# Optimization experiments

Hardware: AMD Instinct MI355X
Metric: run time of the kernel (lower is better)

The kernel has to match this reference:

```python
import jax, jax.numpy as jnp
import numpy as np

N_U, N_P, E = 200000, 50000, 500000
D_U, D_P, H, OUT = 100, 50, 128, 1
BN_EPS = 1e-5


def _lin(k, dout, din):
    s = 1.0 / np.sqrt(din)
    kw, kb = jax.random.split(k)
    W = jax.random.uniform(kw, (dout, din), jnp.float32, -s, s)
    b = jax.random.uniform(kb, (dout,), jnp.float32, -s, s)
    return W, b


def setup_inputs() -> dict:
    key = jax.random.key(0)
    ks = jax.random.split(key, 12)
    x_u = jax.random.normal(ks[0], (N_U, D_U), jnp.float32)
    x_p = jax.random.normal(ks[1], (N_P, D_P), jnp.float32)
    src = jax.random.randint(ks[2], (E,), 0, N_U, jnp.int64) if jax.config.jax_enable_x64 else jax.random.randint(ks[2], (E,), 0, N_U)
    dst = jax.random.randint(ks[3], (E,), N_U, N_U + N_P)
    edge_index = jnp.stack([src, dst]).astype(jnp.int32)
    W_u, b_u = _lin(ks[4], H, D_U)
    W_p, b_p = _lin(ks[5], H, D_P)
    W1l, b1l = _lin(ks[6], H, H)   # SAGEConv lin_l (aggregated neighbors, carries bias)
    W1r, _ = _lin(ks[7], H, H)     # SAGEConv lin_r (root, no bias)
    W2l, b2l = _lin(ks[8], H, H)
    W2r, _ = _lin(ks[9], H, H)
    W_out, b_out = _lin(ks[10], OUT, H)
    return dict(x_u=x_u, x_p=x_p, edge_index=edge_index,
                W_u=W_u, b_u=b_u, W_p=W_p, b_p=b_p,
                W1l=W1l, b1l=b1l, W1r=W1r,
                g1=jnp.ones((H,), jnp.float32), be1=jnp.zeros((H,), jnp.float32),
                W2l=W2l, b2l=b2l, W2r=W2r,
                g2=jnp.ones((H,), jnp.float32), be2=jnp.zeros((H,), jnp.float32),
                W_out=W_out, b_out=b_out)


def reference(x_u, x_p, edge_index, W_u, b_u, W_p, b_p,
              W1l, b1l, W1r, g1, be1, W2l, b2l, W2r, g2, be2,
              W_out, b_out):
    N = x_u.shape[0] + x_p.shape[0]
    # input projections + relu, then concat users/products -> [N, H]
    x = jnp.concatenate([jax.nn.relu(x_u @ W_u.T + b_u),
                         jax.nn.relu(x_p @ W_p.T + b_p)], axis=0)
    # to_undirected: add reversed edges (bipartite => no duplicates)
    src = jnp.concatenate([edge_index[0], edge_index[1]])
    dst = jnp.concatenate([edge_index[1], edge_index[0]])
    deg = jnp.maximum(jax.ops.segment_sum(jnp.ones_like(dst, jnp.float32), dst, num_segments=N), 1.0)

    def sage(h, Wl, bl, Wr):
        # mean aggregation of neighbor features, scatter by dst
        mean = jax.ops.segment_sum(h[src], dst, num_segments=N) / deg[:, None]
        return mean @ Wl.T + bl + h @ Wr.T

    def bn(h, g, b):
        m = h.mean(0)
        v = h.var(0)  # biased variance, as used for normalization in torch BN
        return (h - m) * jax.lax.rsqrt(v + BN_EPS) * g + b

    h1 = jax.nn.relu(bn(sage(x, W1l, b1l, W1r), g1, be1))   # dropout = identity (eval)
    h2 = jax.nn.relu(bn(sage(h1, W2l, b2l, W2r), g2, be2)) + x
    return h2[: x_u.shape[0]] @ W_out.T + b_out
```

## Files before the change

kernel.cpp:

```cpp
#include <hip/hip_runtime.h>
#include <hip/hip_bf16.h>
#include <cstdint>
#include <cstddef>

#define NT   250000
#define NUU  200000
#define NPP  50000
#define EG   500000
#define E2   1000000
#define HD   128
#define NBLK_SCAN 977

#define CNT2_OFF   0ull
#define SPART2_OFF 1000000ull
#define SS2_OFF    1065536ull
#define RPTR2_OFF  1067584ull
#define BSUM2_OFF  2067588ull
#define BMAT2_OFF  2071504ull
#define COL2_OFF   2251728ull
#define X2_OFF     6251728ull
#define R1B_OFF    70251728ull
#define R2B_OFF    134251728ull
#define WS_SPLIT   198251728ull

typedef __hip_bfloat16 bf16;
typedef __attribute__((ext_vector_type(8))) short short8v;
typedef __attribute__((ext_vector_type(4))) float f32x4;

__device__ inline float b2f(short s) { return __builtin_bit_cast(float, ((unsigned)(unsigned short)s) << 16); }
__device__ inline unsigned short f2bf(float f) { return __builtin_bit_cast(unsigned short, __float2bfloat16(f)); }

__global__ __launch_bounds__(256) void k_zero(int* __restrict__ p, int n) {
    for (int i = blockIdx.x * 256 + threadIdx.x; i < n; i += gridDim.x * 256) p[i] = 0;
}

__global__ __launch_bounds__(256) void k_count(const int* __restrict__ ei, int* __restrict__ cnt) {
    for (int e = blockIdx.x * 256 + threadIdx.x; e < EG; e += gridDim.x * 256) {
        int s = ei[e], d = ei[e + EG];
        atomicAdd(&cnt[d], 1);
        atomicAdd(&cnt[s], 1);
    }
}

__global__ __launch_bounds__(256) void k_scan1(const int* __restrict__ cnt, int* __restrict__ bsum) {
    __shared__ int lds[256];
    int i = blockIdx.x * 256 + threadIdx.x;
    int v = (i < NT) ? cnt[i] : 0;
    lds[threadIdx.x] = v; __syncthreads();
    for (int s = 128; s > 0; s >>= 1) {
        if (threadIdx.x < s) lds[threadIdx.x] += lds[threadIdx.x + s];
        __syncthreads();
    }
    if (threadIdx.x == 0) bsum[blockIdx.x] = lds[0];
}

__global__ __launch_bounds__(1024) void k_scan2(int* __restrict__ bsum) {
    __shared__ int lds[1024];
    int i = threadIdx.x;
    int v = (i < NBLK_SCAN) ? bsum[i] : 0;
    lds[i] = v; __syncthreads();
    for (int off = 1; off < 1024; off <<= 1) {
        int t = (i >= off) ? lds[i - off] : 0;
        __syncthreads();
        lds[i] += t;
        __syncthreads();
    }
    if (i < NBLK_SCAN) bsum[i] = lds[i] - v;
}

__global__ __launch_bounds__(256) void k_scan3(const int* __restrict__ cnt, const int* __restrict__ bsum,
                                               int* __restrict__ rp) {
    __shared__ int lds[256];
    int i = blockIdx.x * 256 + threadIdx.x;
    int v = (i < NT) ? cnt[i] : 0;
    lds[threadIdx.x] = v; __syncthreads();
    for (int off = 1; off < 256; off <<= 1) {
        int t = (threadIdx.x >= off) ? lds[threadIdx.x - off] : 0;
        __syncthreads();
        lds[threadIdx.x] += t;
        __syncthreads();
    }
    if (i < NT) rp[i] = bsum[blockIdx.x] + lds[threadIdx.x] - v;
    if (i == 0 && blockIdx.x == 0) rp[NT] = E2;
}

__global__ __launch_bounds__(256) void k_fill(const int* __restrict__ ei, const int* __restrict__ rp,
                                              int* __restrict__ fill, int* __restrict__ col) {
    for (int e = blockIdx.x * 256 + threadIdx.x; e < EG; e += gridDim.x * 256) {
        int s = ei[e], d = ei[e + EG];
        int slot1 = rp[d] + atomicAdd(&fill[d], 1);
        col[slot1] = s;
        int slot2 = rp[s] + atomicAdd(&fill[s], 1);
        col[slot2] = d;
    }
}

__global__ __launch_bounds__(256) void k_wcvt(const float* __restrict__ W1l, const float* __restrict__ W1r,
                                              const float* __restrict__ W2l, const float* __restrict__ W2r,
                                              const float* __restrict__ Wu, const float* __restrict__ Wp,
                                              bf16* __restrict__ B) {
    int i = blockIdx.x * 256 + threadIdx.x;
    if (i < 65536) {
        int layer = i >> 15, rem = i & 32767, o = rem >> 8, k = rem & 255;
        const float* W = layer ? ((k < 128) ? W2l : W2r) : ((k < 128) ? W1l : W1r);
        B[i] = __float2bfloat16(W[o * 128 + (k & 127)]);
    } else if (i < 81920) {
        int rem = i - 65536, o = rem >> 7, k = rem & 127;
        B[i] = __float2bfloat16((k < 100) ? Wu[o * 100 + k] : 0.f);
    } else if (i < 90112) {
        int rem = i - 81920, o = rem >> 6, k = rem & 63;
        B[i] = __float2bfloat16((k < 50) ? Wp[o * 50 + k] : 0.f);
    }
}

template<int DIN, int KPAD>
__device__ __forceinline__ void proj_tile(char* As, const float* __restrict__ in,
                                          const bf16* __restrict__ Bp, const float* __restrict__ bias,
                                          bf16* __restrict__ outp, int nrows, int rowbase, int bid) {
    const int tid = threadIdx.x;
    const int tb = bid * 128;
    constexpr int RSTRIDE = KPAD * 2;
    constexpr int PADE = KPAD - DIN;
    constexpr int PH = PADE / 2;
    constexpr int PPAD = 128 * PH;
    constexpr int PMAIN = 128 * DIN / 2;

    for (int q = tid; q < PPAD; q += 256) {
        int row = q / PH;
        int k = DIN + (q - row * PH) * 2;
        *(unsigned*)(As + row * RSTRIDE + ((((k >> 3) << 4) ^ ((row & 7) << 4)) + (k & 7) * 2)) = 0u;
    }
    for (int q = tid; q < PMAIN; q += 256) {
        int f = q * 2;
        int row = f / DIN, k = f - row * DIN;
        int rg = tb + row; if (rg > nrows - 1) rg = nrows - 1;
        float2 v = *(const float2*)(in + (size_t)rg * DIN + k);
        unsigned u = (unsigned)f2bf(v.x) | ((unsigned)f2bf(v.y) << 16);
        *(unsigned*)(As + row * RSTRIDE + ((((k >> 3) << 4) ^ ((row & 7) << 4)) + (k & 7) * 2)) = u;
    }
    __syncthreads();

    const int lane = tid & 63, wid = tid >> 6;
    const int wr = wid >> 1, wc = wid & 1;
    const int r15 = lane & 15, l4 = lane >> 4;
    constexpr int NKS = KPAD / 32;
    f32x4 acc[4][4] = {};
#pragma unroll
    for (int ks = 0; ks < NKS; ks++) {
        short8v a[4], b[4];
#pragma unroll
        for (int m = 0; m < 4; m++) {
            int rl = wr * 64 + m * 16 + r15;
            a[m] = *(const short8v*)(As + rl * RSTRIDE + ((ks * 64 + l4 * 16) ^ ((rl & 7) << 4)));
        }
#pragma unroll
        for (int n = 0; n < 4; n++) {
            int c = wc * 64 + n * 16 + r15;
            b[n] = *(const short8v*)(Bp + (size_t)c * KPAD + ks * 32 + l4 * 8);
        }
#pragma unroll
        for (int m = 0; m < 4; m++)
#pragma unroll
            for (int n = 0; n < 4; n++)
                acc[m][n] = __builtin_amdgcn_mfma_f32_16x16x32_bf16(a[m], b[n], acc[m][n], 0, 0, 0);
    }
    float bcol[4];
#pragma unroll
    for (int n = 0; n < 4; n++) bcol[n] = bias[wc * 64 + n * 16 + r15];
#pragma unroll
    for (int m = 0; m < 4; m++)
#pragma unroll
        for (int n = 0; n < 4; n++)
#pragma unroll
            for (int g = 0; g < 4; g++) {
                int row = tb + wr * 64 + m * 16 + l4 * 4 + g;
                if (row < nrows) {
                    float v = fmaxf(acc[m][n][g] + bcol[n], 0.f);
                    outp[(size_t)(rowbase + row) * HD + wc * 64 + n * 16 + r15] = __float2bfloat16(v);
                }
            }
}

__global__ __launch_bounds__(256) void k_proj2(const float* __restrict__ xu, const float* __restrict__ xp,
                                               const bf16* __restrict__ Bm, const float* __restrict__ bu,
                                               const float* __restrict__ bp, bf16* __restrict__ X) {
    __shared__ __align__(16) char As[32768];
    if (blockIdx.x < 1563)
        proj_tile<100, 128>(As, xu, Bm + 65536, bu, X, NUU, 0, blockIdx.x);
    else
        proj_tile<50, 64>(As, xp, Bm + 81920, bp, X, NPP, NUU, blockIdx.x - 1563);
}

template<bool NORM>
__global__ __launch_bounds__(256) void k_layer(const bf16* __restrict__ hin, const float* __restrict__ ssv,
                                               const int* __restrict__ rp, const int* __restrict__ col,
                                               const bf16* __restrict__ Bmat, const float* __restrict__ blv,
                                               bf16* __restrict__ outp, float* __restrict__ spart,
                                               int store_n) {
    int g = blockIdx.x / 5, pos = blockIdx.x % 5;
    int tile = (pos < 4) ? (g * 4 + pos) : (1563 + g);
    if (pos < 4 && tile > 1562) return;

    __shared__ __align__(16) char At[32768];
    __shared__ int rpl[129];
    __shared__ int ctr;
    const int tid = threadIdx.x;
    const int tb = tile * 128;

    if (tid < 129) rpl[tid] = rp[min(tb + tid, NT)];
    if (tid == 255) ctr = 0;
    __syncthreads();

    const int lane = tid & 63;
    const int l8 = tid & 7;
    const int fo = l8 * 8;
    float sva[8], tva[8], svb[8], tvb[8];
    if (NORM) {
#pragma unroll
        for (int j = 0; j < 8; j++) {
            sva[j] = ssv[fo + j];      tva[j] = ssv[HD + fo + j];
            svb[j] = ssv[64 + fo + j]; tvb[j] = ssv[HD + 64 + fo + j];
        }
    }
    for (;;) {
        int nl = 0;
        if (l8 == 0) nl = atomicAdd(&ctr, 1);
        nl = __shfl(nl, lane & 56);
        if (nl >= 128) break;
        int s0 = rpl[nl], s1 = rpl[nl + 1];
        float a[8] = {}, b[8] = {};
        for (int p = s0; p < s1; p += 4) {
            int i1 = min(p + 1, s1 - 1), i2 = min(p + 2, s1 - 1), i3 = min(p + 3, s1 - 1);
            int c0 = col[p], c1 = col[i1], c2 = col[i2], c3 = col[i3];
            const bf16* r0p = hin + (size_t)c0 * HD + fo;
            const bf16* r1p = hin + (size_t)c1 * HD + fo;
            const bf16* r2p = hin + (size_t)c2 * HD + fo;
            const bf16* r3p = hin + (size_t)c3 * HD + fo;
            short8v uA0 = *(const short8v*)r0p, uB0 = *(const short8v*)(r0p + 64);
            short8v uA1 = *(const short8v*)r1p, uB1 = *(const short8v*)(r1p + 64);
            short8v uA2 = *(const short8v*)r2p, uB2 = *(const short8v*)(r2p + 64);
            short8v uA3 = *(const short8v*)r3p, uB3 = *(const short8v*)(r3p + 64);
            float m1 = (p + 1 < s1) ? 1.f : 0.f;
            float m2 = (p + 2 < s1) ? 1.f : 0.f;
            float m3 = (p + 3 < s1) ? 1.f : 0.f;
#pragma unroll
            for (int j = 0; j < 8; j++) {
                float vA0 = b2f(uA0[j]), vA1 = b2f(uA1[j]), vA2 = b2f(uA2[j]), vA3 = b2f(uA3[j]);
                float vB0 = b2f(uB0[j]), vB1 = b2f(uB1[j]), vB2 = b2f(uB2[j]), vB3 = b2f(uB3[j]);
                if (NORM) {
                    vA0 = fmaxf(fmaf(vA0, sva[j], tva[j]), 0.f);
                    vA1 = fmaxf(fmaf(vA1, sva[j], tva[j]), 0.f);
                    vA2 = fmaxf(fmaf(vA2, sva[j], tva[j]), 0.f);
                    vA3 = fmaxf(fmaf(vA3, sva[j], tva[j]), 0.f);
                    vB0 = fmaxf(fmaf(vB0, svb[j], tvb[j]), 0.f);
                    vB1 = fmaxf(fmaf(vB1, svb[j], tvb[j]), 0.f);
                    vB2 = fmaxf(fmaf(vB2, svb[j], tvb[j]), 0.f);
                    vB3 = fmaxf(fmaf(vB3, svb[j], tvb[j]), 0.f);
                }
                a[j] += vA0 + m1 * vA1 + m2 * vA2 + m3 * vA3;
                b[j] += vB0 + m1 * vB1 + m2 * vB2 + m3 * vB3;
            }
        }
        float inv = 1.f / (float)max(s1 - s0, 1);
        short8v wa, wb;
#pragma unroll
        for (int j = 0; j < 8; j++) { wa[j] = (short)f2bf(a[j] * inv); wb[j] = (short)f2bf(b[j] * inv); }
        *(short8v*)(At + nl * 256 + ((l8 * 16) ^ ((nl & 7) << 4))) = wa;
        *(short8v*)(At + nl * 256 + (((8 + l8) * 16) ^ ((nl & 7) << 4))) = wb;
    }

    const int seg = tid & 15, r0 = tid >> 4;
    const int sfo = seg * 8;
    short8v vh[8];
#pragma unroll
    for (int it = 0; it < 8; it++) {
        int row = r0 + it * 16;
        int r = tb + row; if (r > NT - 1) r = NT - 1;
        vh[it] = *(const short8v*)(hin + (size_t)r * HD + sfo);
    }
    __syncthreads();

    const int wid = tid >> 6;
    const int wr = wid >> 1, wc = wid & 1;
    const int r15 = lane & 15, l4 = lane >> 4;
    f32x4 acc[4][4] = {};
#pragma unroll
    for (int ks = 0; ks < 4; ks++) {
        short8v a[4], b[4];
#pragma unroll
        for (int m = 0; m < 4; m++) {
            int rl = wr * 64 + m * 16 + r15;
            a[m] = *(const short8v*)(At + rl * 256 + ((ks * 64 + l4 * 16) ^ ((rl & 7) << 4)));
        }
#pragma unroll
        for (int n = 0; n < 4; n++) {
            int c = wc * 64 + n * 16 + r15;
            b[n] = *(const short8v*)(Bmat + (size_t)c * 256 + ks * 32 + l4 * 8);
        }
#pragma unroll
        for (int m = 0; m < 4; m++)
#pragma unroll
            for (int n = 0; n < 4; n++)
                acc[m][n] = __builtin_amdgcn_mfma_f32_16x16x32_bf16(a[m], b[n], acc[m][n], 0, 0, 0);
    }
    __syncthreads();

    if (NORM) {
        float sv2[8], tv2[8];
#pragma unroll
        for (int j = 0; j < 8; j++) { sv2[j] = ssv[sfo + j]; tv2[j] = ssv[HD + sfo + j]; }
#pragma unroll
        for (int it = 0; it < 8; it++) {
#pragma unroll
            for (int j = 0; j < 8; j++) {
                float f = b2f(vh[it][j]);
                vh[it][j] = (short)f2bf(fmaxf(fmaf(f, sv2[j], tv2[j]), 0.f));
            }
        }
    }
#pragma unroll
    for (int it = 0; it < 8; it++) {
        int row = r0 + it * 16;
        *(short8v*)(At + row * 256 + ((seg * 16) ^ ((row & 7) << 4))) = vh[it];
    }
    __syncthreads();

#pragma unroll
    for (int ks = 0; ks < 4; ks++) {
        short8v a[4], b[4];
#pragma unroll
        for (int m = 0; m < 4; m++) {
            int rl = wr * 64 + m * 16 + r15;
            a[m] = *(const short8v*)(At + rl * 256 + ((ks * 64 + l4 * 16) ^ ((rl & 7) << 4)));
        }
#pragma unroll
        for (int n = 0; n < 4; n++) {
            int c = wc * 64 + n * 16 + r15;
            b[n] = *(const short8v*)(Bmat + (size_t)c * 256 + (ks + 4) * 32 + l4 * 8);
        }
#pragma unroll
        for (int m = 0; m < 4; m++)
#pragma unroll
            for (int n = 0; n < 4; n++)
                acc[m][n] = __builtin_amdgcn_mfma_f32_16x16x32_bf16(a[m], b[n], acc[m][n], 0, 0, 0);
    }

    float bcol[4];
#pragma unroll
    for (int n = 0; n < 4; n++) bcol[n] = blv[wc * 64 + n * 16 + r15];
    float ls[4] = {0.f, 0.f, 0.f, 0.f}, lq[4] = {0.f, 0.f, 0.f, 0.f};
#pragma unroll
    for (int m = 0; m < 4; m++)
#pragma unroll
        for (int n = 0; n < 4; n++)
#pragma unroll
            for (int gg = 0; gg < 4; gg++) {
                int row = tb + wr * 64 + m * 16 + l4 * 4 + gg;
                float v = acc[m][n][gg] + bcol[n];
                if (row < NT) { ls[n] += v; lq[n] += v * v; }
                if (row < store_n)
                    outp[(size_t)row * HD + wc * 64 + n * 16 + r15] = __float2bfloat16(v);
            }
    int part = (tile & 31) * 256;
#pragma unroll
    for (int n = 0; n < 4; n++) {
        float s = ls[n], q2 = lq[n];
        s  += __shfl_xor(s, 16);  s  += __shfl_xor(s, 32);
        q2 += __shfl_xor(q2, 16); q2 += __shfl_xor(q2, 32);
        if (l4 == 0) {
            atomicAdd(&spart[part + wc * 64 + n * 16 + r15], s);
            atomicAdd(&spart[part + 128 + wc * 64 + n * 16 + r15], q2);
        }
    }
}

__global__ void k_fin(const float* __restrict__ sp, const float* __restrict__ g,
                      const float* __restrict__ be, float* __restrict__ ssout) {
    int j = threadIdx.x;
    float m = 0.f, q = 0.f;
    for (int i = 0; i < 32; i++) { m += sp[i * 256 + j]; q += sp[i * 256 + 128 + j]; }
    m *= (1.f / (float)NT);
    q = q * (1.f / (float)NT) - m * m;
    float s = g[j] * rsqrtf(q + 1e-5f);
    ssout[j] = s;
    ssout[HD + j] = be[j] - m * s;
}

__global__ __launch_bounds__(256) void k_out(const bf16* __restrict__ r2, const float* __restrict__ ss,
                                             const bf16* __restrict__ x, const float* __restrict__ wout,
                                             const float* __restrict__ bout, float* __restrict__ outp) {
    int lane = threadIdx.x & 63;
    int wv = (blockIdx.x * blockDim.x + threadIdx.x) >> 6;
    int nwv = (gridDim.x * blockDim.x) >> 6;
    int g16 = lane >> 4, l16 = lane & 15;
    int fo = l16 * 8;
    float s8[8], t8[8], w8[8];
#pragma unroll
    for (int j = 0; j < 8; j++) {
        s8[j] = ss[fo + j]; t8[j] = ss[HD + fo + j]; w8[j] = wout[fo + j];
    }
    float bo = bout[0];
    for (int r0 = wv * 4; r0 < NUU; r0 += nwv * 4) {
        int row = r0 + g16;
        short8v a  = *(const short8v*)(r2 + (size_t)row * HD + fo);
        short8v xx = *(const short8v*)(x  + (size_t)row * HD + fo);
        float acc = 0.f;
#pragma unroll
        for (int j = 0; j < 8; j++) {
            float h = fmaxf(fmaf(b2f(a[j]), s8[j], t8[j]), 0.f) + b2f(xx[j]);
            acc += h * w8[j];
        }
        acc += __shfl_xor(acc, 1);
        acc += __shfl_xor(acc, 2);
        acc += __shfl_xor(acc, 4);
        acc += __shfl_xor(acc, 8);
        if (l16 == 0) outp[row] = acc + bo;
    }
}

extern "C" void kernel_launch(void* const* d_in, const int* in_sizes, int n_in,
                              void* d_out, int out_size, void* d_ws, size_t ws_size,
                              hipStream_t stream) {
    const float* x_u = (const float*)d_in[0];
    const float* x_p = (const float*)d_in[1];
    const int*   ei  = (const int*)d_in[2];
    const float* W_u = (const float*)d_in[3];
    const float* b_u = (const float*)d_in[4];
    const float* W_p = (const float*)d_in[5];
    const float* b_p = (const float*)d_in[6];
    const float* W1l = (const float*)d_in[7];
    const float* b1l = (const float*)d_in[8];
    const float* W1r = (const float*)d_in[9];
    const float* g1  = (const float*)d_in[10];
    const float* be1 = (const float*)d_in[11];
    const float* W2l = (const float*)d_in[12];
    const float* b2l = (const float*)d_in[13];
    const float* W2r = (const float*)d_in[14];
    const float* g2  = (const float*)d_in[15];
    const float* be2 = (const float*)d_in[16];
    const float* Wout = (const float*)d_in[17];
    const float* bout = (const float*)d_in[18];
    float* out = (float*)d_out;
    char* ws = (char*)d_ws;

    if (ws_size < WS_SPLIT) {
        k_zero<<<512, 256, 0, stream>>>((int*)d_out, out_size);
        return;
    }

    int*  cnt    = (int*)(ws + CNT2_OFF);
    float* spart = (float*)(ws + SPART2_OFF);
    float* ssbuf = (float*)(ws + SS2_OFF);
    int*  rp     = (int*)(ws + RPTR2_OFF);
    int*  bsum   = (int*)(ws + BSUM2_OFF);
    bf16* Bmat   = (bf16*)(ws + BMAT2_OFF);
    int*  col    = (int*)(ws + COL2_OFF);
    bf16* X      = (bf16*)(ws + X2_OFF);
    bf16* R1     = (bf16*)(ws + R1B_OFF);
    bf16* R2     = (bf16*)(ws + R2B_OFF);

    k_zero<<<1043, 256, 0, stream>>>(cnt, 266896);
    k_wcvt<<<352, 256, 0, stream>>>(W1l, W1r, W2l, W2r, W_u, W_p, Bmat);

    k_count<<<1024, 256, 0, stream>>>(ei, cnt);
    k_scan1<<<NBLK_SCAN, 256, 0, stream>>>(cnt, bsum);
    k_scan2<<<1, 1024, 0, stream>>>(bsum);
    k_scan3<<<NBLK_SCAN, 256, 0, stream>>>(cnt, bsum, rp);
    k_zero<<<977, 256, 0, stream>>>(cnt, NT);
    k_fill<<<1024, 256, 0, stream>>>(ei, rp, cnt, col);

    k_proj2<<<1954, 256, 0, stream>>>(x_u, x_p, Bmat, b_u, b_p, X);

    k_layer<false><<<1955, 256, 0, stream>>>(X, nullptr, rp, col, Bmat, b1l, R1, spart, NT);
    k_fin<<<1, 128, 0, stream>>>(spart, g1, be1, ssbuf);

    k_layer<true><<<1955, 256, 0, stream>>>(R1, ssbuf, rp, col, Bmat + 32768, b2l, R2, spart + 8192, NUU);
    k_fin<<<1, 128, 0, stream>>>(spart + 8192, g2, be2, ssbuf + 256);

    k_out<<<2048, 256, 0, stream>>>(R2, ssbuf + 256, X, Wout, bout, out);
}
```

Baseline: 416.2 us.

## Make SAGE layer kernel wave-independent with per-wave row strips

Each wave now owns a 32-row strip of the tile and does its own gather, mean aggregation and full 128-column MFMA GEMM on that strip. The shared atomic work counter and all block-wide __syncthreads are replaced by wave barriers, so waves no longer wait on each other. The root-feature load is hoisted to the start to overlap with the gather. In exchange, nodes are statically assigned to waves, so skewed degrees can unbalance the waves. Each wave also reloads all of Bmat itself, raising B-operand traffic per wave.

```diff
diff --git a/kernel.cpp b/kernel.cpp
--- a/kernel.cpp
+++ b/kernel.cpp
@@ -202,17 +202,21 @@
     if (pos < 4 && tile > 1562) return;
 
     __shared__ __align__(16) char At[32768];
-    __shared__ int rpl[129];
-    __shared__ int ctr;
     const int tid = threadIdx.x;
-    const int tb = tile * 128;
-
-    if (tid < 129) rpl[tid] = rp[min(tb + tid, NT)];
-    if (tid == 255) ctr = 0;
-    __syncthreads();
-
-    const int lane = tid & 63;
-    const int l8 = tid & 7;
+    const int lane = tid & 63, w = tid >> 6;
+    const int rowbase = tile * 128 + w * 32;
+    char* strip = At + w * 8192;
+
+    const int seg = lane & 15, l4 = lane >> 4;
+    const int sfo = seg * 8;
+    short8v vh[8];
+#pragma unroll
+    for (int it = 0; it < 8; it++) {
+        int r = rowbase + it * 4 + l4; if (r > NT - 1) r = NT - 1;
+        vh[it] = *(const short8v*)(hin + (size_t)r * HD + sfo);
+    }
+
+    const int g8 = lane >> 3, l8 = lane & 7;
     const int fo = l8 * 8;
     float sva[8], tva[8], svb[8], tvb[8];
     if (NORM) {
@@ -222,12 +226,12 @@
             svb[j] = ssv[64 + fo + j]; tvb[j] = ssv[HD + 64 + fo + j];
         }
     }
-    for (;;) {
-        int nl = 0;
-        if (l8 == 0) nl = atomicAdd(&ctr, 1);
-        nl = __shfl(nl, lane & 56);
-        if (nl >= 128) break;
-        int s0 = rpl[nl], s1 = rpl[nl + 1];
+#pragma unroll 1
+    for (int q = 0; q < 4; q++) {
+        int rr = q * 8 + g8;
+        int node = rowbase + rr;
+        int s0 = 0, s1 = 0;
+        if (node < NT) { s0 = rp[node]; s1 = rp[node + 1]; }
         float a[8] = {}, b[8] = {};
         for (int p = s0; p < s1; p += 4) {
             int i1 = min(p + 1, s1 - 1), i2 = min(p + 2, s1 - 1), i3 = min(p + 3, s1 - 1);
@@ -265,45 +269,26 @@
         short8v wa, wb;
 #pragma unroll
         for (int j = 0; j < 8; j++) { wa[j] = (short)f2bf(a[j] * inv); wb[j] = (short)f2bf(b[j] * inv); }
-        *(short8v*)(At + nl * 256 + ((l8 * 16) ^ ((nl & 7) << 4))) = wa;
-        *(short8v*)(At + nl * 256 + (((8 + l8) * 16) ^ ((nl & 7) << 4))) = wb;
-    }
-
-    const int seg = tid & 15, r0 = tid >> 4;
-    const int sfo = seg * 8;
-    short8v vh[8];
-#pragma unroll
-    for (int it = 0; it < 8; it++) {
-        int row = r0 + it * 16;
-        int r = tb + row; if (r > NT - 1) r = NT - 1;
-        vh[it] = *(const short8v*)(hin + (size_t)r * HD + sfo);
-    }
-    __syncthreads();
-
-    const int wid = tid >> 6;
-    const int wr = wid >> 1, wc = wid & 1;
-    const int r15 = lane & 15, l4 = lane >> 4;
-    f32x4 acc[4][4] = {};
+        *(short8v*)(strip + rr * 256 + ((l8 * 16) ^ ((rr & 7) << 4))) = wa;
+        *(short8v*)(strip + rr * 256 + (((8 + l8) * 16) ^ ((rr & 7) << 4))) = wb;
+    }
+    __builtin_amdgcn_wave_barrier();
+
+    const int r15 = lane & 15;
+    f32x4 acc[2][8] = {};
 #pragma unroll
     for (int ks = 0; ks < 4; ks++) {
-        short8v a[4], b[4];
-#pragma unroll
-        for (int m = 0; m < 4; m++) {
-            int rl = wr * 64 + m * 16 + r15;
-            a[m] = *(const short8v*)(At + rl * 256 + ((ks * 64 + l4 * 16) ^ ((rl & 7) << 4)));
-        }
-#pragma unroll
-        for (int n = 0; n < 4; n++) {
-            int c = wc * 64 + n * 16 + r15;
-            b[n] = *(const short8v*)(Bmat + (size_t)c * 256 + ks * 32 + l4 * 8);
-        }
-#pragma unroll
-        for (int m = 0; m < 4; m++)
-#pragma unroll
-            for (int n = 0; n < 4; n++)
-                acc[m][n] = __builtin_amdgcn_mfma_f32_16x16x32_bf16(a[m], b[n], acc[m][n], 0, 0, 0);
-    }
-    __syncthreads();
+        int kb = (ks * 64 + l4 * 16) ^ ((r15 & 7) << 4);
+        short8v a0 = *(const short8v*)(strip + r15 * 256 + kb);
+        short8v a1 = *(const short8v*)(strip + (16 + r15) * 256 + kb);
+#pragma unroll
+        for (int n = 0; n < 8; n++) {
+            short8v b = *(const short8v*)(Bmat + (size_t)(n * 16 + r15) * 256 + ks * 32 + l4 * 8);
+            acc[0][n] = __builtin_amdgcn_mfma_f32_16x16x32_bf16(a0, b, acc[0][n], 0, 0, 0);
+            acc[1][n] = __builtin_amdgcn_mfma_f32_16x16x32_bf16(a1, b, acc[1][n], 0, 0, 0);
+        }
+    }
+    __builtin_amdgcn_wave_barrier();
 
     if (NORM) {
         float sv2[8], tv2[8];
@@ -320,56 +305,44 @@
     }
 #pragma unroll
     for (int it = 0; it < 8; it++) {
-        int row = r0 + it * 16;
-        *(short8v*)(At + row * 256 + ((seg * 16) ^ ((row & 7) << 4))) = vh[it];
-    }
-    __syncthreads();
+        int rr = it * 4 + l4;
+        *(short8v*)(strip + rr * 256 + ((seg * 16) ^ ((rr & 7) << 4))) = vh[it];
+    }
+    __builtin_amdgcn_wave_barrier();
 
 #pragma unroll
     for (int ks = 0; ks < 4; ks++) {
-        short8v a[4], b[4];
-#pragma unroll
-        for (int m = 0; m < 4; m++) {
-            int rl = wr * 64 + m * 16 + r15;
-            a[m] = *(const short8v*)(At + rl * 256 + ((ks * 64 + l4 * 16) ^ ((rl & 7) << 4)));
-        }
-#pragma unroll
-        for (int n = 0; n < 4; n++) {
-            int c = wc * 64 + n * 16 + r15;
-            b[n] = *(const short8v*)(Bmat + (size_t)c * 256 + (ks + 4) * 32 + l4 * 8);
-        }
-#pragma unroll
-        for (int m = 0; m < 4; m++)
-#pragma unroll
-            for (int n = 0; n < 4; n++)
-                acc[m][n] = __builtin_amdgcn_mfma_f32_16x16x32_bf16(a[m], b[n], acc[m][n], 0, 0, 0);
-    }
-
-    float bcol[4];
-#pragma unroll
-    for (int n = 0; n < 4; n++) bcol[n] = blv[wc * 64 + n * 16 + r15];
-    float ls[4] = {0.f, 0.f, 0.f, 0.f}, lq[4] = {0.f, 0.f, 0.f, 0.f};
-#pragma unroll
-    for (int m = 0; m < 4; m++)
-#pragma unroll
-        for (int n = 0; n < 4; n++)
+        int kb = (ks * 64 + l4 * 16) ^ ((r15 & 7) << 4);
+        short8v a0 = *(const short8v*)(strip + r15 * 256 + kb);
+        short8v a1 = *(const short8v*)(strip + (16 + r15) * 256 + kb);
+#pragma unroll
+        for (int n = 0; n < 8; n++) {
+            short8v b = *(const short8v*)(Bmat + (size_t)(n * 16 + r15) * 256 + (ks + 4) * 32 + l4 * 8);
+            acc[0][n] = __builtin_amdgcn_mfma_f32_16x16x32_bf16(a0, b, acc[0][n], 0, 0, 0);
+            acc[1][n] = __builtin_amdgcn_mfma_f32_16x16x32_bf16(a1, b, acc[1][n], 0, 0, 0);
+        }
+    }
+
+    int part = (tile & 31) * 256;
+#pragma unroll
+    for (int n = 0; n < 8; n++) {
+        float bc = blv[n * 16 + r15];
+        float ls = 0.f, lq = 0.f;
+#pragma unroll
+        for (int h = 0; h < 2; h++)
 #pragma unroll
             for (int gg = 0; gg < 4; gg++) {
-                int row = tb + wr * 64 + m * 16 + l4 * 4 + gg;
-                float v = acc[m][n][gg] + bcol[n];
-                if (row < NT) { ls[n] += v; lq[n] += v * v; }
+                int row = rowbase + h * 16 + l4 * 4 + gg;
+                float v = acc[h][n][gg] + bc;
+                if (row < NT) { ls += v; lq += v * v; }
                 if (row < store_n)
-                    outp[(size_t)row * HD + wc * 64 + n * 16 + r15] = __float2bfloat16(v);
+                    outp[(size_t)row * HD + n * 16 + r15] = __float2bfloat16(v);
             }
-    int part = (tile & 31) * 256;
-#pragma unroll
-    for (int n = 0; n < 4; n++) {
-        float s = ls[n], q2 = lq[n];
-        s  += __shfl_xor(s, 16);  s  += __shfl_xor(s, 32);
-        q2 += __shfl_xor(q2, 16); q2 += __shfl_xor(q2, 32);
+        ls += __shfl_xor(ls, 16); ls += __shfl_xor(ls, 32);
+        lq += __shfl_xor(lq, 16); lq += __shfl_xor(lq, 32);
         if (l4 == 0) {
-            atomicAdd(&spart[part + wc * 64 + n * 16 + r15], s);
-            atomicAdd(&spart[part + 128 + wc * 64 + n * 16 + r15], q2);
+            atomicAdd(&spart[part + n * 16 + r15], ls);
+            atomicAdd(&spart[part + 128 + n * 16 + r15], lq);
         }
     }
 }
```

Result: slower. 542.5 us (+30.3%).
